# Kernel tuning notes

Measured on AMD Instinct MI355X. Metric: run time of the kernel, lower is better.

Reference implementation:

```python
import jax, jax.numpy as jnp
import numpy as np

NUM_HEADS = 12
OT_REG = 0.1
SINKHORN_ITERS = 10
DIAG_VAL = 1e3


def setup_inputs() -> dict:
    key = jax.random.key(0)
    k1, k2, k3 = jax.random.split(key, 3)
    B, N, C = 64, 256, 768
    x = jax.random.normal(k1, (B, N, C), dtype=jnp.float32)
    w_qkv = jax.random.normal(k2, (3 * C, C), dtype=jnp.float32) * (C ** -0.5)
    w_proj = jax.random.normal(k3, (C, C), dtype=jnp.float32) * (C ** -0.5)
    b_proj = jnp.zeros((C,), dtype=jnp.float32)
    return {"x": x, "w_qkv": w_qkv, "w_proj": w_proj, "b_proj": b_proj}


def _sot(q):
    # q: [B, H, N, hd] -> self-optimal-transport plan [B, H, N, N]
    N = q.shape[-2]
    qn = q / (jnp.linalg.norm(q, axis=-1, keepdims=True) + 1e-8)
    C = 1.0 - jnp.einsum('bhnd,bhmd->bhnm', qn, qn)          # cosine cost
    eye = jnp.eye(N, dtype=bool)
    C = jnp.where(eye, DIAG_VAL, C)                            # mask diagonal
    log_K = -C / OT_REG
    log_marg = -jnp.log(jnp.float32(N))                        # uniform r = c = 1/N
    log_v = jnp.zeros(q.shape[:2] + (N,), dtype=q.dtype)
    for _ in range(SINKHORN_ITERS):
        log_u = log_marg - jax.nn.logsumexp(log_K + log_v[..., None, :], axis=-1)
        log_v = log_marg - jax.nn.logsumexp(log_K + log_u[..., :, None], axis=-2)
    log_T = log_u[..., :, None] + log_K + log_v[..., None, :]
    z = jnp.exp(log_T)
    z = z / jnp.max(z, axis=(-2, -1), keepdims=True)           # max_scale per sample/head
    z = jnp.where(eye, 1.0, z)                                 # diagonal set to 1
    return z


def reference(x, w_qkv, w_proj, b_proj):
    B, N, C = x.shape
    H = NUM_HEADS
    hd = C // H
    scale = hd ** -0.5
    qkv = jnp.einsum('bnc,oc->bno', x, w_qkv)                  # [B, N, 3C]
    qkv = qkv.reshape(B, N, 3, H, hd).transpose(2, 0, 3, 1, 4)  # [3, B, H, N, hd]
    q, k, v = qkv[0], qkv[1], qkv[2]
    attn = _sot(q)                                              # [B, H, N, N]
    attn = jax.nn.softmax(attn * scale, axis=-1)               # dropout = identity (eval)
    out = jnp.einsum('bhnm,bhmd->bhnd', attn, v)
    out = out.transpose(0, 2, 1, 3).reshape(B, N, C)
    out = jnp.einsum('bnc,oc->bno', out, w_proj) + b_proj
    return out
```

## Files before the change

### kernel.cpp

```cpp
#include <hip/hip_runtime.h>

typedef unsigned short u16;
typedef unsigned int   u32;
typedef __attribute__((ext_vector_type(8))) short bf16x8;
typedef __attribute__((ext_vector_type(4))) float f32x4;

__device__ __forceinline__ u16 f2bf(float f) {
    u32 u = __float_as_uint(f);
    u += 0x7fffu + ((u >> 16) & 1u);
    return (u16)(u >> 16);
}
__device__ __forceinline__ float bf2f(u16 s) {
    return __uint_as_float(((u32)s) << 16);
}
__device__ __forceinline__ u32 pack2bf(float f0, float f1) {
    return (u32)f2bf(f0) | ((u32)f2bf(f1) << 16);
}

__device__ __forceinline__ void gload_lds16(const void* g, void* l) {
    __builtin_amdgcn_global_load_lds(
        (const __attribute__((address_space(1))) u32*)g,
        (__attribute__((address_space(3))) u32*)l, 16, 0, 0);
}

__global__ __launch_bounds__(256)
void conv_bf16(const float* __restrict__ src, u16* __restrict__ dst, int n8)
{
    const int i = blockIdx.x * 256 + threadIdx.x;
    if (i < n8) {
        const float4 a = ((const float4*)src)[2*i];
        const float4 b = ((const float4*)src)[2*i + 1];
        ((uint4*)dst)[i] = make_uint4(pack2bf(a.x,a.y), pack2bf(a.z,a.w),
                                      pack2bf(b.x,b.y), pack2bf(b.z,b.w));
    }
}

__global__ __launch_bounds__(256)
void conv_wqv(const float* __restrict__ w, u16* __restrict__ dst)
{
    const int i = blockIdx.x * 256 + threadIdx.x;
    const int row = i / 96;
    const int cc  = (i - row * 96) * 8;
    const int srow = row + (row >= 768 ? 768 : 0);
    const float4 a = *(const float4*)&w[(size_t)srow*768 + cc];
    const float4 b = *(const float4*)&w[(size_t)srow*768 + cc + 4];
    *(uint4*)&dst[(size_t)row*768 + cc] =
        make_uint4(pack2bf(a.x,a.y), pack2bf(a.z,a.w), pack2bf(b.x,b.y), pack2bf(b.z,b.w));
}

__device__ __forceinline__ void mfma_gemm_core(
    const char* __restrict__ Arow0,
    const char* __restrict__ Brow0,
    u16* As, u16* Bs, const int tid, f32x4 acc[4][4])
{
    const int l  = tid & 63, w = tid >> 6;
    const int wr = w >> 1,  wc = w & 1;
    char* Asb = (char*)As;
    char* Bsb = (char*)Bs;
    const int co = 16 * ((l & 7) ^ (l >> 3));
    const size_t rstep = (size_t)(l >> 3) * 1536;
    const int rsw = (l & 7) << 4;

    for (int k0 = 0; k0 < 1536; k0 += 128) {
        #pragma unroll
        for (int i = 0; i < 4; ++i) {
            const int rb = i*32 + w*8;
            gload_lds16(Arow0 + (size_t)rb*1536 + rstep + k0 + co, Asb + i*4096 + w*1024);
            gload_lds16(Brow0 + (size_t)rb*1536 + rstep + k0 + co, Bsb + i*4096 + w*1024);
        }
        __syncthreads();
        bf16x8 af[2][4], bfr[2][4];
        #pragma unroll
        for (int kk = 0; kk < 2; ++kk) {
            const int coff = (kk*64 + ((l >> 4) << 4)) ^ rsw;
            #pragma unroll
            for (int mi = 0; mi < 4; ++mi) {
                const int rowA = wr*64 + mi*16 + (l & 15);
                af[kk][mi]  = *(const bf16x8*)(Asb + rowA*128 + coff);
                const int rowB = wc*64 + mi*16 + (l & 15);
                bfr[kk][mi] = *(const bf16x8*)(Bsb + rowB*128 + coff);
            }
        }
        #pragma unroll
        for (int mi = 0; mi < 4; ++mi)
            #pragma unroll
            for (int nj = 0; nj < 4; ++nj) {
                acc[mi][nj] = __builtin_amdgcn_mfma_f32_16x16x32_bf16(
                                  af[0][mi], bfr[0][nj], acc[mi][nj], 0, 0, 0);
                acc[mi][nj] = __builtin_amdgcn_mfma_f32_16x16x32_bf16(
                                  af[1][mi], bfr[1][nj], acc[mi][nj], 0, 0, 0);
            }
        __syncthreads();
    }
}

__global__ __launch_bounds__(256)
void gemm_qkv_mfma(const u16* __restrict__ xbf, const u16* __restrict__ wqv,
                   u16* __restrict__ qnbf, u16* __restrict__ vbfT)
{
    __shared__ u16 As[128*64];
    __shared__ u16 Bs[128*64];
    const int m0 = blockIdx.x * 128;
    const int bj = blockIdx.y;
    const int tid = threadIdx.x;
    f32x4 acc[4][4];
    #pragma unroll
    for (int i = 0; i < 4; ++i)
        #pragma unroll
        for (int j = 0; j < 4; ++j) acc[i][j] = (f32x4){0.f,0.f,0.f,0.f};

    mfma_gemm_core((const char*)xbf + (size_t)m0*1536,
                   (const char*)wqv + (size_t)bj*128*1536,
                   As, Bs, tid, acc);

    const int l = tid & 63, w = tid >> 6;
    const int wr = w >> 1, wc = w & 1;
    const int rbase = m0 + wr*64 + ((l >> 4) << 2);
    if (bj < 6) {
        const int h = 2*bj + wc;
        #pragma unroll
        for (int mi = 0; mi < 4; ++mi)
            #pragma unroll
            for (int rr = 0; rr < 4; ++rr) {
                float s =      acc[mi][0][rr]*acc[mi][0][rr];
                s = fmaf(acc[mi][1][rr], acc[mi][1][rr], s);
                s = fmaf(acc[mi][2][rr], acc[mi][2][rr], s);
                s = fmaf(acc[mi][3][rr], acc[mi][3][rr], s);
                #pragma unroll
                for (int off = 1; off < 16; off <<= 1) s += __shfl_xor(s, off);
                const float inv = 1.0f / (sqrtf(s) + 1e-8f);
                const int m = rbase + mi*16 + rr;
                const int b_ = m >> 8, n_ = m & 255;
                u16* row = qnbf + ((((size_t)b_*12 + h) << 8) + n_)*64;
                #pragma unroll
                for (int nj = 0; nj < 4; ++nj)
                    row[nj*16 + (l & 15)] = f2bf(acc[mi][nj][rr] * inv);
            }
    } else {
        const int colb = (bj - 6)*128 + wc*64;
        #pragma unroll
        for (int mi = 0; mi < 4; ++mi)
            #pragma unroll
            for (int nj = 0; nj < 4; ++nj) {
                const int col = colb + nj*16 + (l & 15);
                const int h = col >> 6, d = col & 63;
                const int m = rbase + mi*16;
                const int b_ = m >> 8, n_ = m & 255;
                uint2 o = make_uint2(pack2bf(acc[mi][nj][0], acc[mi][nj][1]),
                                     pack2bf(acc[mi][nj][2], acc[mi][nj][3]));
                *(uint2*)&vbfT[(((size_t)b_*12 + h)*64 + d)*256 + n_] = o;
            }
    }
}

__global__ __launch_bounds__(256)
void gemm_proj_mfma(const u16* __restrict__ ctxb, const u16* __restrict__ wpb,
                    const float* __restrict__ bias, float* __restrict__ out)
{
    __shared__ u16 As[128*64];
    __shared__ u16 Bs[128*64];
    const int m0 = blockIdx.x * 128;
    const int n0 = blockIdx.y * 128;
    const int tid = threadIdx.x;
    f32x4 acc[4][4];
    #pragma unroll
    for (int i = 0; i < 4; ++i)
        #pragma unroll
        for (int j = 0; j < 4; ++j) acc[i][j] = (f32x4){0.f,0.f,0.f,0.f};

    mfma_gemm_core((const char*)ctxb + (size_t)m0*1536,
                   (const char*)wpb + (size_t)n0*1536,
                   As, Bs, tid, acc);

    const int l = tid & 63, w = tid >> 6;
    const int wr = w >> 1, wc = w & 1;
    const int rbase = m0 + wr*64 + ((l >> 4) << 2);
    #pragma unroll
    for (int mi = 0; mi < 4; ++mi)
        #pragma unroll
        for (int nj = 0; nj < 4; ++nj) {
            const int col = n0 + wc*64 + nj*16 + (l & 15);
            const float bv = bias[col];
            #pragma unroll
            for (int rr = 0; rr < 4; ++rr) {
                const int m = rbase + mi*16 + rr;
                out[(size_t)m*768 + col] = acc[mi][nj][rr] + bv;
            }
        }
}

__global__ __launch_bounds__(256)
void cost_kernel(const u16* __restrict__ qnbf, u16* __restrict__ Kmat)
{
    __shared__ u16 Qa[128*64];
    __shared__ u16 Qb[128*64];
    const int bh = blockIdx.y;
    const int tr = (blockIdx.x >> 1) * 128;
    const int tc = (blockIdx.x & 1) * 128;
    const char* qb = (const char*)(qnbf + (size_t)bh * 16384);
    const int tid = threadIdx.x;
    const int l = tid & 63, w = tid >> 6;
    const int wr = w >> 1, wc = w & 1;

    {
        const int co = ((l & 7) ^ (l >> 3)) << 4;
        const int rl = l >> 3;
        #pragma unroll
        for (int i = 0; i < 4; ++i) {
            const int ch = i*4 + w;
            gload_lds16(qb + (size_t)(tr + ch*8 + rl)*128 + co, (char*)Qa + ch*1024);
            gload_lds16(qb + (size_t)(tc + ch*8 + rl)*128 + co, (char*)Qb + ch*1024);
        }
    }
    __syncthreads();

    f32x4 acc[4][4];
    #pragma unroll
    for (int i = 0; i < 4; ++i)
        #pragma unroll
        for (int j = 0; j < 4; ++j) acc[i][j] = (f32x4){0.f,0.f,0.f,0.f};

    bf16x8 af[2][4], bfr[2][4];
    #pragma unroll
    for (int kk = 0; kk < 2; ++kk) {
        const int kb = kk*64 + ((l >> 4) << 4);
        #pragma unroll
        for (int f = 0; f < 4; ++f) {
            const int ra = wr*64 + f*16 + (l & 15);
            af[kk][f]  = *(const bf16x8*)((char*)Qa + ra*128 + (kb ^ ((ra & 7) << 4)));
            const int rb = wc*64 + f*16 + (l & 15);
            bfr[kk][f] = *(const bf16x8*)((char*)Qb + rb*128 + (kb ^ ((rb & 7) << 4)));
        }
    }
    #pragma unroll
    for (int mi = 0; mi < 4; ++mi)
        #pragma unroll
        for (int nj = 0; nj < 4; ++nj) {
            acc[mi][nj] = __builtin_amdgcn_mfma_f32_16x16x32_bf16(
                              af[0][mi], bfr[0][nj], acc[mi][nj], 0, 0, 0);
            acc[mi][nj] = __builtin_amdgcn_mfma_f32_16x16x32_bf16(
                              af[1][mi], bfr[1][nj], acc[mi][nj], 0, 0, 0);
        }

    u16* Kb = Kmat + (size_t)bh * 65536;
    #pragma unroll
    for (int mi = 0; mi < 4; ++mi)
        #pragma unroll
        for (int nj = 0; nj < 4; ++nj) {
            const int gr0 = tr + wr*64 + mi*16 + ((l >> 4) << 2);
            const int gc  = tc + wc*64 + nj*16 + (l & 15);
            #pragma unroll
            for (int rr = 0; rr < 4; ++rr) {
                const int gr = gr0 + rr;
                const float s = acc[mi][nj][rr];
                const float km = (gr == gc) ? 0.f : __expf(fmaf(10.f, s, -10.f));
                Kb[(size_t)gr * 256 + gc] = f2bf(km);
            }
        }
}

__global__ __launch_bounds__(512, 4)
void sinkhorn_kernel(const u16* __restrict__ Kmat, float* __restrict__ ubuf,
                     float* __restrict__ vbuf, float* __restrict__ tmaxbuf)
{
    __shared__ __align__(16) float ys[256];
    __shared__ __align__(16) float xv[256];
    __shared__ __align__(16) float usave[256];
    __shared__ __align__(16) u16   xbf[256];
    __shared__ float pmax[8];
    const int bh  = blockIdx.x;
    const int tid = threadIdx.x;
    const int l = tid & 63, w = tid >> 6;
    const int rowb = w * 32;
    const char* Kg = (const char*)(Kmat + (size_t)bh * 65536);

    bf16x8 kf[2][8];
    {
        const char* kb0 = Kg + (size_t)(rowb + (l & 15)) * 512 + ((l >> 4) << 4);
        #pragma unroll
        for (int t = 0; t < 2; ++t)
            #pragma unroll
            for (int ks = 0; ks < 8; ++ks)
                kf[t][ks] = *(const bf16x8*)(kb0 + t*8192 + ks*64);
    }
    if (tid < 256) { xv[tid] = 1.0f; xbf[tid] = 0x3f80; }
    __syncthreads();

    for (int it = 0; it < 20; ++it) {
        f32x4 a0 = {0.f,0.f,0.f,0.f}, a1 = {0.f,0.f,0.f,0.f};
        #pragma unroll
        for (int ks = 0; ks < 8; ++ks) {
            const bf16x8 xf = *(const bf16x8*)((const char*)xbf + ks*64 + ((l >> 4) << 4));
            a0 = __builtin_amdgcn_mfma_f32_16x16x32_bf16(kf[0][ks], xf, a0, 0, 0, 0);
            a1 = __builtin_amdgcn_mfma_f32_16x16x32_bf16(kf[1][ks], xf, a1, 0, 0, 0);
        }
        if ((l & 15) == 0) {
            const int r0 = rowb + ((l >> 4) << 2);
            *(float4*)&ys[r0]      = make_float4(a0[0], a0[1], a0[2], a0[3]);
            *(float4*)&ys[r0 + 16] = make_float4(a1[0], a1[1], a1[2], a1[3]);
        }
        __syncthreads();
        if (tid < 256) {
            const float xn = 0.00390625f / ys[tid];
            if (it == 18) usave[tid] = xn;
            xv[tid]  = xn;
            xbf[tid] = f2bf(xn);
        }
        __syncthreads();
    }

    float mx = 0.f;
    {
        const float u0 = usave[rowb + (l & 15)];
        const float u1 = usave[rowb + 16 + (l & 15)];
        #pragma unroll
        for (int ks = 0; ks < 8; ++ks) {
            const float4 va = *(const float4*)&xv[ks*32 + ((l >> 4) << 3)];
            const float4 vb4 = *(const float4*)&xv[ks*32 + ((l >> 4) << 3) + 4];
            const float vv[8] = {va.x, va.y, va.z, va.w, vb4.x, vb4.y, vb4.z, vb4.w};
            #pragma unroll
            for (int j = 0; j < 8; ++j) {
                mx = fmaxf(mx, u0 * bf2f((u16)kf[0][ks][j]) * vv[j]);
                mx = fmaxf(mx, u1 * bf2f((u16)kf[1][ks][j]) * vv[j]);
            }
        }
    }
    #pragma unroll
    for (int off = 32; off > 0; off >>= 1) mx = fmaxf(mx, __shfl_xor(mx, off));
    if (l == 0) pmax[w] = mx;
    __syncthreads();
    if (tid < 256) {
        ubuf[bh * 256 + tid] = usave[tid];
        vbuf[bh * 256 + tid] = xv[tid];
    }
    if (tid == 0) {
        float m = pmax[0];
        #pragma unroll
        for (int i = 1; i < 8; ++i) m = fmaxf(m, pmax[i]);
        tmaxbuf[bh] = m;
    }
}

__global__ __launch_bounds__(256)
void softpv_kernel(const u16* __restrict__ Kmat, const u16* __restrict__ vbfT,
                   const float* __restrict__ ubuf, const float* __restrict__ vbuf,
                   const float* __restrict__ tmaxbuf, u16* __restrict__ ctxc)
{
    __shared__ u16 Vt[64*256];
    __shared__ u16 Pl[256*64];
    __shared__ float vmf[256];
    __shared__ float sinv[256];
    const int bh = blockIdx.x;
    const int b_ = bh / 12, h_ = bh - b_*12;
    const int tid = threadIdx.x;
    const int l = tid & 63, w = tid >> 6;

    {
        const char* src = (const char*)(vbfT + (size_t)bh * 16384);
        char* dst = (char*)Vt;
        const int s = l & 31;
        #pragma unroll
        for (int i = 0; i < 8; ++i) {
            const int d = i*8 + w*2 + (l >> 5);
            gload_lds16(src + d*512 + ((s ^ (d & 7)) << 4), dst + i*4096 + w*1024);
        }
    }
    vmf[tid] = vbuf[bh*256 + tid];
    const float an = ubuf[bh*256 + tid] * (1.0f / tmaxbuf[bh]) * 0.125f;
    const u16* Krow = Kmat + (size_t)bh*65536 + (size_t)tid*256;
    __syncthreads();

    f32x4 acc[4][4];
    #pragma unroll
    for (int i = 0; i < 4; ++i)
        #pragma unroll
        for (int j = 0; j < 4; ++j) acc[i][j] = (f32x4){0.f,0.f,0.f,0.f};
    float psum = 0.f;
    char* prow = (char*)Pl + tid*128;
    const int nsw = tid & 7;

    #pragma unroll
    for (int mc = 0; mc < 4; ++mc) {
        const uint4* kr = (const uint4*)(Krow + mc*64);
        #pragma unroll
        for (int i = 0; i < 8; ++i) {
            const uint4 raw = kr[i];
            const float4 va = *(const float4*)&vmf[mc*64 + i*8];
            const float4 vbq = *(const float4*)&vmf[mc*64 + i*8 + 4];
            float p[8];
            p[0] = __expf(an * bf2f((u16)(raw.x & 0xffffu)) * va.x);
            p[1] = __expf(an * bf2f((u16)(raw.x >> 16))     * va.y);
            p[2] = __expf(an * bf2f((u16)(raw.y & 0xffffu)) * va.z);
            p[3] = __expf(an * bf2f((u16)(raw.y >> 16))     * va.w);
            p[4] = __expf(an * bf2f((u16)(raw.z & 0xffffu)) * vbq.x);
            p[5] = __expf(an * bf2f((u16)(raw.z >> 16))     * vbq.y);
            p[6] = __expf(an * bf2f((u16)(raw.w & 0xffffu)) * vbq.z);
            p[7] = __expf(an * bf2f((u16)(raw.w >> 16))     * vbq.w);
            const int dj = tid - mc*64 - i*8;
            if (dj >= 0 && dj < 8) p[dj] = 1.13314845f;
            psum += ((p[0]+p[1]) + (p[2]+p[3])) + ((p[4]+p[5]) + (p[6]+p[7]));
            uint4 pw = make_uint4(pack2bf(p[0],p[1]), pack2bf(p[2],p[3]),
                                  pack2bf(p[4],p[5]), pack2bf(p[6],p[7]));
            *(uint4*)(prow + ((i ^ nsw) << 4)) = pw;
        }
        #pragma unroll
        for (int kk = 0; kk < 2; ++kk) {
            bf16x8 afr[4], bfr[4];
            const int kb = kk*64 + ((l >> 4) << 4);
            #pragma unroll
            for (int f = 0; f < 4; ++f) {
                const int d = f*16 + (l & 15);
                afr[f] = *(const bf16x8*)((char*)Vt + d*512 + ((mc*128 + kb) ^ ((d & 7) << 4)));
                const int n = w*64 + f*16 + (l & 15);
                bfr[f] = *(const bf16x8*)((char*)Pl + n*128 + (kb ^ ((n & 7) << 4)));
            }
            #pragma unroll
            for (int mi = 0; mi < 4; ++mi)
                #pragma unroll
                for (int nj = 0; nj < 4; ++nj)
                    acc[mi][nj] = __builtin_amdgcn_mfma_f32_16x16x32_bf16(
                                      afr[mi], bfr[nj], acc[mi][nj], 0, 0, 0);
        }
    }
    sinv[tid] = 1.0f / psum;
    __syncthreads();
    u16* outp = ctxc + ((size_t)b_*256)*768 + h_*64;
    #pragma unroll
    for (int nj = 0; nj < 4; ++nj) {
        const int n = w*64 + nj*16 + (l & 15);
        const float is = sinv[n];
        #pragma unroll
        for (int mi = 0; mi < 4; ++mi) {
            const int d0 = mi*16 + ((l >> 4) << 2);
            uint2 o = make_uint2(pack2bf(acc[mi][nj][0]*is, acc[mi][nj][1]*is),
                                 pack2bf(acc[mi][nj][2]*is, acc[mi][nj][3]*is));
            *(uint2*)&outp[(size_t)n*768 + d0] = o;
        }
    }
}

extern "C" void kernel_launch(void* const* d_in, const int* in_sizes, int n_in,
                              void* d_out, int out_size, void* d_ws, size_t ws_size,
                              hipStream_t stream)
{
    (void)in_sizes; (void)n_in; (void)out_size; (void)ws_size;
    const float* x      = (const float*)d_in[0];
    const float* w_qkv  = (const float*)d_in[1];
    const float* w_proj = (const float*)d_in[2];
    const float* b_proj = (const float*)d_in[3];
    float* out = (float*)d_out;

    char* w = (char*)d_ws;
    u16*   xbf  = (u16*)  (w);
    u16*   wqv  = (u16*)  (w + 25165824);
    u16*   wpb  = (u16*)  (w + 27525120);
    u16*   qnbf = (u16*)  (w + 28704768);
    u16*   vbfT = (u16*)  (w + 79036416);
    u16*   ctxc = (u16*)  (w + 104202240);
    float* ub   = (float*)(w + 129368064);
    float* vb   = (float*)(w + 130154496);
    float* tmx  = (float*)(w + 130940928);
    u16*   Km   = (u16*)  (w + 130944000);

    conv_bf16       <<<dim3(6144),    256, 0, stream>>>(x, xbf, 1572864);
    conv_wqv        <<<dim3(576),     256, 0, stream>>>(w_qkv, wqv);
    conv_bf16       <<<dim3(288),     256, 0, stream>>>(w_proj, wpb, 73728);
    gemm_qkv_mfma   <<<dim3(128, 12), 256, 0, stream>>>(xbf, wqv, qnbf, vbfT);
    cost_kernel     <<<dim3(4, 768),  256, 0, stream>>>(qnbf, Km);
    sinkhorn_kernel <<<dim3(768),     512, 0, stream>>>(Km, ub, vb, tmx);
    softpv_kernel   <<<dim3(768),     256, 0, stream>>>(Km, vbfT, ub, vb, tmx, ctxc);
    gemm_proj_mfma  <<<dim3(128, 6),  256, 0, stream>>>(ctxc, wpb, b_proj, out);
}
```

Baseline: 224.9 us.

## Fuse Sinkhorn iterations with softmax and PV into one kernel

Merges the Sinkhorn kernel and the softmax·V kernel. The exponentiated probabilities are computed from the K fragments already held in registers, overwritten in place, and fed straight into MFMAs against a V tile loaded into LDS at kernel start. This removes a second 32 MB read of the Kmat matrix, the u/v/tmax round trip through global memory, one kernel launch, and the P staging in LDS. In exchange it adds 32 KB of LDS and more register pressure, so the occupancy hint drops from 4 to 3 blocks per CU.

Result: slower. 262.5 us (+16.7%).

```diff
diff --git a/kernel.cpp b/kernel.cpp
--- a/kernel.cpp
+++ b/kernel.cpp
@@ -259,20 +259,33 @@
         }
 }
 
-__global__ __launch_bounds__(512, 4)
-void sinkhorn_kernel(const u16* __restrict__ Kmat, float* __restrict__ ubuf,
-                     float* __restrict__ vbuf, float* __restrict__ tmaxbuf)
-{
+__global__ __launch_bounds__(512, 3)
+void sinkhorn_attn_kernel(const u16* __restrict__ Kmat, const u16* __restrict__ vbfT,
+                          u16* __restrict__ ctxc)
+{
+    __shared__ u16 Vt[64*256];
     __shared__ __align__(16) float ys[256];
     __shared__ __align__(16) float xv[256];
     __shared__ __align__(16) float usave[256];
     __shared__ __align__(16) u16   xbf[256];
     __shared__ float pmax[8];
     const int bh  = blockIdx.x;
+    const int b_ = bh / 12, h_ = bh - b_*12;
     const int tid = threadIdx.x;
     const int l = tid & 63, w = tid >> 6;
     const int rowb = w * 32;
     const char* Kg = (const char*)(Kmat + (size_t)bh * 65536);
+
+    {
+        const char* src = (const char*)(vbfT + (size_t)bh * 16384);
+        char* dst = (char*)Vt;
+        const int s = l & 31;
+        #pragma unroll
+        for (int i = 0; i < 4; ++i) {
+            const int d = i*16 + w*2 + (l >> 5);
+            gload_lds16(src + d*512 + ((s ^ (d & 7)) << 4), dst + i*8192 + w*1024);
+        }
+    }
 
     bf16x8 kf[2][8];
     {
@@ -309,14 +322,15 @@
         __syncthreads();
     }
 
-    float mx = 0.f;
     {
+        float mx = 0.f;
         const float u0 = usave[rowb + (l & 15)];
         const float u1 = usave[rowb + 16 + (l & 15)];
         #pragma unroll
         for (int ks = 0; ks < 8; ++ks) {
-            const float4 va = *(const float4*)&xv[ks*32 + ((l >> 4) << 3)];
-            const float4 vb4 = *(const float4*)&xv[ks*32 + ((l >> 4) << 3) + 4];
+            const int mbase = ks*32 + ((l >> 4) << 3);
+            const float4 va  = *(const float4*)&xv[mbase];
+            const float4 vb4 = *(const float4*)&xv[mbase + 4];
             const float vv[8] = {va.x, va.y, va.z, va.w, vb4.x, vb4.y, vb4.z, vb4.w};
             #pragma unroll
             for (int j = 0; j < 8; ++j) {
@@ -324,116 +338,78 @@
                 mx = fmaxf(mx, u1 * bf2f((u16)kf[1][ks][j]) * vv[j]);
             }
         }
-    }
-    #pragma unroll
-    for (int off = 32; off > 0; off >>= 1) mx = fmaxf(mx, __shfl_xor(mx, off));
-    if (l == 0) pmax[w] = mx;
+        #pragma unroll
+        for (int off = 32; off > 0; off >>= 1) mx = fmaxf(mx, __shfl_xor(mx, off));
+        if (l == 0) pmax[w] = mx;
+    }
     __syncthreads();
-    if (tid < 256) {
-        ubuf[bh * 256 + tid] = usave[tid];
-        vbuf[bh * 256 + tid] = xv[tid];
-    }
-    if (tid == 0) {
-        float m = pmax[0];
-        #pragma unroll
-        for (int i = 1; i < 8; ++i) m = fmaxf(m, pmax[i]);
-        tmaxbuf[bh] = m;
-    }
-}
-
-__global__ __launch_bounds__(256)
-void softpv_kernel(const u16* __restrict__ Kmat, const u16* __restrict__ vbfT,
-                   const float* __restrict__ ubuf, const float* __restrict__ vbuf,
-                   const float* __restrict__ tmaxbuf, u16* __restrict__ ctxc)
-{
-    __shared__ u16 Vt[64*256];
-    __shared__ u16 Pl[256*64];
-    __shared__ float vmf[256];
-    __shared__ float sinv[256];
-    const int bh = blockIdx.x;
-    const int b_ = bh / 12, h_ = bh - b_*12;
-    const int tid = threadIdx.x;
-    const int l = tid & 63, w = tid >> 6;
-
+    float tm = pmax[0];
+    #pragma unroll
+    for (int i = 1; i < 8; ++i) tm = fmaxf(tm, pmax[i]);
+    const float itmax = 1.0f / tm;
+
+    float psum[2] = {0.f, 0.f};
     {
-        const char* src = (const char*)(vbfT + (size_t)bh * 16384);
-        char* dst = (char*)Vt;
-        const int s = l & 31;
-        #pragma unroll
-        for (int i = 0; i < 8; ++i) {
-            const int d = i*8 + w*2 + (l >> 5);
-            gload_lds16(src + d*512 + ((s ^ (d & 7)) << 4), dst + i*4096 + w*1024);
-        }
-    }
-    vmf[tid] = vbuf[bh*256 + tid];
-    const float an = ubuf[bh*256 + tid] * (1.0f / tmaxbuf[bh]) * 0.125f;
-    const u16* Krow = Kmat + (size_t)bh*65536 + (size_t)tid*256;
-    __syncthreads();
-
-    f32x4 acc[4][4];
-    #pragma unroll
-    for (int i = 0; i < 4; ++i)
-        #pragma unroll
-        for (int j = 0; j < 4; ++j) acc[i][j] = (f32x4){0.f,0.f,0.f,0.f};
-    float psum = 0.f;
-    char* prow = (char*)Pl + tid*128;
-    const int nsw = tid & 7;
-
-    #pragma unroll
-    for (int mc = 0; mc < 4; ++mc) {
-        const uint4* kr = (const uint4*)(Krow + mc*64);
-        #pragma unroll
-        for (int i = 0; i < 8; ++i) {
-            const uint4 raw = kr[i];
-            const float4 va = *(const float4*)&vmf[mc*64 + i*8];
-            const float4 vbq = *(const float4*)&vmf[mc*64 + i*8 + 4];
-            float p[8];
-            p[0] = __expf(an * bf2f((u16)(raw.x & 0xffffu)) * va.x);
-            p[1] = __expf(an * bf2f((u16)(raw.x >> 16))     * va.y);
-            p[2] = __expf(an * bf2f((u16)(raw.y & 0xffffu)) * va.z);
-            p[3] = __expf(an * bf2f((u16)(raw.y >> 16))     * va.w);
-            p[4] = __expf(an * bf2f((u16)(raw.z & 0xffffu)) * vbq.x);
-            p[5] = __expf(an * bf2f((u16)(raw.z >> 16))     * vbq.y);
-            p[6] = __expf(an * bf2f((u16)(raw.w & 0xffffu)) * vbq.z);
-            p[7] = __expf(an * bf2f((u16)(raw.w >> 16))     * vbq.w);
-            const int dj = tid - mc*64 - i*8;
-            if (dj >= 0 && dj < 8) p[dj] = 1.13314845f;
-            psum += ((p[0]+p[1]) + (p[2]+p[3])) + ((p[4]+p[5]) + (p[6]+p[7]));
-            uint4 pw = make_uint4(pack2bf(p[0],p[1]), pack2bf(p[2],p[3]),
-                                  pack2bf(p[4],p[5]), pack2bf(p[6],p[7]));
-            *(uint4*)(prow + ((i ^ nsw) << 4)) = pw;
-        }
-        #pragma unroll
-        for (int kk = 0; kk < 2; ++kk) {
-            bf16x8 afr[4], bfr[4];
-            const int kb = kk*64 + ((l >> 4) << 4);
-            #pragma unroll
-            for (int f = 0; f < 4; ++f) {
-                const int d = f*16 + (l & 15);
-                afr[f] = *(const bf16x8*)((char*)Vt + d*512 + ((mc*128 + kb) ^ ((d & 7) << 4)));
-                const int n = w*64 + f*16 + (l & 15);
-                bfr[f] = *(const bf16x8*)((char*)Pl + n*128 + (kb ^ ((n & 7) << 4)));
-            }
-            #pragma unroll
-            for (int mi = 0; mi < 4; ++mi)
+        const float an[2] = { usave[rowb + (l & 15)] * itmax * 0.125f,
+                              usave[rowb + 16 + (l & 15)] * itmax * 0.125f };
+        #pragma unroll
+        for (int t = 0; t < 2; ++t) {
+            const int rown = rowb + t*16 + (l & 15);
+            #pragma unroll
+            for (int ks = 0; ks < 8; ++ks) {
+                const int mbase = ks*32 + ((l >> 4) << 3);
+                const float4 va  = *(const float4*)&xv[mbase];
+                const float4 vb4 = *(const float4*)&xv[mbase + 4];
+                const float vv[8] = {va.x, va.y, va.z, va.w, vb4.x, vb4.y, vb4.z, vb4.w};
+                float p[8];
                 #pragma unroll
-                for (int nj = 0; nj < 4; ++nj)
-                    acc[mi][nj] = __builtin_amdgcn_mfma_f32_16x16x32_bf16(
-                                      afr[mi], bfr[nj], acc[mi][nj], 0, 0, 0);
-        }
-    }
-    sinv[tid] = 1.0f / psum;
-    __syncthreads();
+                for (int j = 0; j < 8; ++j)
+                    p[j] = __expf(an[t] * bf2f((u16)kf[t][ks][j]) * vv[j]);
+                const int dj = rown - mbase;
+                if (dj >= 0 && dj < 8) p[dj] = 1.13314845f;
+                psum[t] += ((p[0]+p[1]) + (p[2]+p[3])) + ((p[4]+p[5]) + (p[6]+p[7]));
+                bf16x8 pf;
+                #pragma unroll
+                for (int j = 0; j < 8; ++j) pf[j] = (short)f2bf(p[j]);
+                kf[t][ks] = pf;
+            }
+            psum[t] += __shfl_xor(psum[t], 16);
+            psum[t] += __shfl_xor(psum[t], 32);
+        }
+    }
+
+    f32x4 acc[2][4];
+    #pragma unroll
+    for (int t = 0; t < 2; ++t)
+        #pragma unroll
+        for (int dt = 0; dt < 4; ++dt) acc[t][dt] = (f32x4){0.f,0.f,0.f,0.f};
+    #pragma unroll
+    for (int ks = 0; ks < 8; ++ks) {
+        bf16x8 vf[4];
+        const int bc = ks*64 + ((l >> 4) << 4);
+        #pragma unroll
+        for (int dt = 0; dt < 4; ++dt) {
+            const int d = dt*16 + (l & 15);
+            vf[dt] = *(const bf16x8*)((char*)Vt + d*512 + (bc ^ ((d & 7) << 4)));
+        }
+        #pragma unroll
+        for (int t = 0; t < 2; ++t)
+            #pragma unroll
+            for (int dt = 0; dt < 4; ++dt)
+                acc[t][dt] = __builtin_amdgcn_mfma_f32_16x16x32_bf16(
+                                 vf[dt], kf[t][ks], acc[t][dt], 0, 0, 0);
+    }
+
     u16* outp = ctxc + ((size_t)b_*256)*768 + h_*64;
     #pragma unroll
-    for (int nj = 0; nj < 4; ++nj) {
-        const int n = w*64 + nj*16 + (l & 15);
-        const float is = sinv[n];
-        #pragma unroll
-        for (int mi = 0; mi < 4; ++mi) {
-            const int d0 = mi*16 + ((l >> 4) << 2);
-            uint2 o = make_uint2(pack2bf(acc[mi][nj][0]*is, acc[mi][nj][1]*is),
-                                 pack2bf(acc[mi][nj][2]*is, acc[mi][nj][3]*is));
+    for (int t = 0; t < 2; ++t) {
+        const int n = rowb + t*16 + (l & 15);
+        const float is = 1.0f / psum[t];
+        #pragma unroll
+        for (int dt = 0; dt < 4; ++dt) {
+            const int d0 = dt*16 + ((l >> 4) << 2);
+            uint2 o = make_uint2(pack2bf(acc[t][dt][0]*is, acc[t][dt][1]*is),
+                                 pack2bf(acc[t][dt][2]*is, acc[t][dt][3]*is));
             *(uint2*)&outp[(size_t)n*768 + d0] = o;
         }
     }
@@ -457,17 +433,13 @@
     u16*   qnbf = (u16*)  (w + 28704768);
     u16*   vbfT = (u16*)  (w + 79036416);
     u16*   ctxc = (u16*)  (w + 104202240);
-    float* ub   = (float*)(w + 129368064);
-    float* vb   = (float*)(w + 130154496);
-    float* tmx  = (float*)(w + 130940928);
     u16*   Km   = (u16*)  (w + 130944000);
 
-    conv_bf16       <<<dim3(6144),    256, 0, stream>>>(x, xbf, 1572864);
-    conv_wqv        <<<dim3(576),     256, 0, stream>>>(w_qkv, wqv);
-    conv_bf16       <<<dim3(288),     256, 0, stream>>>(w_proj, wpb, 73728);
-    gemm_qkv_mfma   <<<dim3(128, 12), 256, 0, stream>>>(xbf, wqv, qnbf, vbfT);
-    cost_kernel     <<<dim3(4, 768),  256, 0, stream>>>(qnbf, Km);
-    sinkhorn_kernel <<<dim3(768),     512, 0, stream>>>(Km, ub, vb, tmx);
-    softpv_kernel   <<<dim3(768),     256, 0, stream>>>(Km, vbfT, ub, vb, tmx, ctxc);
-    gemm_proj_mfma  <<<dim3(128, 6),  256, 0, stream>>>(ctxc, wpb, b_proj, out);
-}
+    conv_bf16          <<<dim3(6144),    256, 0, stream>>>(x, xbf, 1572864);
+    conv_wqv           <<<dim3(576),     256, 0, stream>>>(w_qkv, wqv);
+    conv_bf16          <<<dim3(288),     256, 0, stream>>>(w_proj, wpb, 73728);
+    gemm_qkv_mfma      <<<dim3(128, 12), 256, 0, stream>>>(xbf, wqv, qnbf, vbfT);
+    cost_kernel        <<<dim3(4, 768),  256, 0, stream>>>(qnbf, Km);
+    sinkhorn_attn_kernel<<<dim3(768),    512, 0, stream>>>(Km, vbfT, ctxc);
+    gemm_proj_mfma     <<<dim3(128, 6),  256, 0, stream>>>(ctxc, wpb, b_proj, out);
+}
```
